# Kernel optimization log

Hardware: AMD Instinct MI355X
Metric: run time of the kernel (lower is better)

## Reference

```python
import jax, jax.numpy as jnp
import numpy as np

N_NODES = 100000
N_EDGES = 3200000
F_IN = 128
F_HID = 16
F_OUT = 1


def setup_inputs() -> dict:
    key = jax.random.key(0)
    ks = jax.random.split(key, 8)
    x = jax.random.normal(ks[0], (N_NODES, F_IN), dtype=jnp.float32)
    src = jax.random.randint(ks[1], (N_EDGES,), 0, N_NODES, dtype=jnp.int32)
    dst = jax.random.randint(ks[2], (N_EDGES,), 0, N_NODES, dtype=jnp.int32)
    edge_w = jax.random.uniform(ks[3], (N_EDGES,), dtype=jnp.float32)
    W0 = jax.random.normal(ks[4], (F_IN, F_HID), dtype=jnp.float32) / np.sqrt(F_IN)
    b0 = jnp.zeros((F_HID,), dtype=jnp.float32)
    W1 = jax.random.normal(ks[5], (F_HID, F_OUT), dtype=jnp.float32) / np.sqrt(F_HID)
    b1 = jnp.zeros((F_OUT,), dtype=jnp.float32)
    return {"x": x, "src": src, "dst": dst, "edge_w": edge_w,
            "W0": W0, "b0": b0, "W1": W1, "b1": b1}


def _spmm(src, dst, edge_w, h):
    # sparse A (COO) @ dense h: gather rows at src, weight, scatter-add to dst
    msgs = h[src] * edge_w[:, None]            # [E, F]
    return jax.ops.segment_sum(msgs, dst, num_segments=N_NODES)  # [N, F]


def reference(x, src, dst, edge_w, W0, b0, W1, b1):
    # GCNConv layer 0: relu(A @ (x @ W0) + b0)
    z0 = x @ W0                                 # [N, 16] linear transform first
    h = jax.nn.relu(_spmm(src, dst, edge_w, z0) + b0)
    # (Dropout is identity at inference)
    # GCNConv layer 1: sigmoid(A @ (h @ W1) + b1)
    z1 = h @ W1                                 # [N, 1]
    out = jax.nn.sigmoid(_spmm(src, dst, edge_w, z1) + b1)
    return out
```

## Files before the change

kernel.cpp:

```cpp
#include <hip/hip_runtime.h>

#define N_NODES 100000
#define N_EDGES 3200000
#define F_IN 128
#define F_HID 16

#define BK_LG 7
#define BK_NODES 128
#define NB ((N_NODES + BK_NODES - 1) / BK_NODES)
#define BCAPF 4736
#define CLG 10
#define CNODES 1024
#define NBC ((N_NODES + CNODES - 1) / CNODES)
#define NBC_P 128
#define BCAPC 34816
#define CPB2 9
#define CHUNK2 4096
#define CHUNK1 2048
#define NCH1 ((N_EDGES + CHUNK1 - 1) / CHUNK1)
#define NXB ((N_NODES + 63) / 64)
#define CUR_STRIDE 16

__device__ __forceinline__ unsigned short f2bf_rne(float f) {
    unsigned u = __float_as_uint(f);
    u += 0x7FFFu + ((u >> 16) & 1u);
    return (unsigned short)(u >> 16);
}

__global__ __launch_bounds__(256) void k_pre(const float* __restrict__ x,
                                             const float* __restrict__ W0,
                                             unsigned short* __restrict__ z0b,
                                             const int* __restrict__ src,
                                             const int* __restrict__ dst,
                                             const float* __restrict__ ew,
                                             int* __restrict__ cursorC,
                                             int2* __restrict__ ebinC) {
    __shared__ __align__(16) char smem[24832];
    const int tid = threadIdx.x;

    if ((blockIdx.x & 1) == 0) {
        const int xb = blockIdx.x >> 1;
        if (xb >= NXB) return;
        unsigned short* xsb = (unsigned short*)smem;
        float* w0s = (float*)(smem + 16640);
        for (int i = tid; i < F_IN * F_HID; i += 256) w0s[i] = W0[i];
        const int row0 = xb * 64;
        for (int i = tid; i < 64 * 32; i += 256) {
            int r = i >> 5, c4 = i & 31;
            float4 v = make_float4(0.f, 0.f, 0.f, 0.f);
            int row = row0 + r;
            if (row < N_NODES) v = ((const float4*)(x + (size_t)row * F_IN))[c4];
            *(ushort2*)(xsb + r * 130 + c4 * 4)     = make_ushort2(f2bf_rne(v.x), f2bf_rne(v.y));
            *(ushort2*)(xsb + r * 130 + c4 * 4 + 2) = make_ushort2(f2bf_rne(v.z), f2bf_rne(v.w));
        }
        __syncthreads();
        const int r  = tid & 63;
        const int cg = tid >> 6;
        float a0 = 0.f, a1 = 0.f, a2 = 0.f, a3 = 0.f;
        #pragma unroll 4
        for (int k = 0; k < F_IN; k += 2) {
            unsigned u = *(const unsigned*)(xsb + r * 130 + k);
            float xv0 = __uint_as_float(u << 16);
            float xv1 = __uint_as_float(u & 0xFFFF0000u);
            const float* wr0 = w0s + k * F_HID + cg * 4;
            const float* wr1 = wr0 + F_HID;
            a0 = fmaf(xv0, wr0[0], a0); a1 = fmaf(xv0, wr0[1], a1);
            a2 = fmaf(xv0, wr0[2], a2); a3 = fmaf(xv0, wr0[3], a3);
            a0 = fmaf(xv1, wr1[0], a0); a1 = fmaf(xv1, wr1[1], a1);
            a2 = fmaf(xv1, wr1[2], a2); a3 = fmaf(xv1, wr1[3], a3);
        }
        int row = row0 + r;
        if (row < N_NODES) {
            ushort4 p = make_ushort4(f2bf_rne(a0), f2bf_rne(a1),
                                     f2bf_rne(a2), f2bf_rne(a3));
            *(ushort4*)(z0b + (size_t)row * F_HID + cg * 4) = p;
        }
    } else {
        const int ch = blockIdx.x >> 1;
        if (ch >= NCH1) return;
        int2* stage = (int2*)smem;
        unsigned char* sbid = (unsigned char*)(smem + 16384);
        int* cnt  = (int*)(smem + 18432);
        int* excl = (int*)(smem + 18944);
        int* run  = (int*)(smem + 19456);
        int* gb   = (int*)(smem + 19968);
        int* alw  = (int*)(smem + 20480);
        int* wtot = (int*)(smem + 20992);
        const int e0  = ch * CHUNK1;
        const int nch = min(CHUNK1, N_EDGES - e0);

        for (int i = tid; i < NBC_P; i += 256) cnt[i] = 0;
        __syncthreads();

        const int EPT1 = CHUNK1 / 256;
        int es[8], eb[8], edl[8]; float ww[8];
        #pragma unroll
        for (int k = 0; k < EPT1; ++k) {
            int idx = k * 256 + tid;
            if (idx < nch) {
                int e = e0 + idx;
                int d = dst[e];
                es[k]  = src[e];
                ww[k]  = ew[e];
                eb[k]  = d >> CLG;
                edl[k] = d & (CNODES - 1);
                atomicAdd(&cnt[eb[k]], 1);
            } else {
                eb[k] = -1;
            }
        }
        __syncthreads();

        {
            const int lane = tid & 63;
            int inc = 0, dv_ = 0;
            if (tid < NBC_P) {
                dv_ = cnt[tid];
                inc = dv_;
                #pragma unroll
                for (int off = 1; off < 64; off <<= 1) {
                    int t = __shfl_up(inc, off);
                    if (lane >= off) inc += t;
                }
                if (lane == 63) wtot[tid >> 6] = inc;
            }
            __syncthreads();
            if (tid < NBC_P) {
                int base = (tid >= 64) ? wtot[0] : 0;
                excl[tid] = base + inc - dv_;
            }
        }
        __syncthreads();

        if (tid < NBC) {
            int c = cnt[tid];
            if (c > 0) {
                int old = atomicAdd(&cursorC[tid * CUR_STRIDE], c);
                int a = BCAPC - old;
                a = (a < 0) ? 0 : ((a > c) ? c : a);
                alw[tid] = a;
                gb[tid]  = tid * BCAPC + old;
            } else {
                alw[tid] = 0;
                gb[tid]  = tid * BCAPC;
            }
            run[tid] = 0;
        }
        __syncthreads();

        #pragma unroll
        for (int k = 0; k < EPT1; ++k) {
            if (eb[k] >= 0) {
                int b = eb[k];
                int p = excl[b] + atomicAdd(&run[b], 1);
                stage[p] = make_int2(__float_as_int(ww[k]), es[k] | (edl[k] << 17));
                sbid[p]  = (unsigned char)b;
            }
        }
        __syncthreads();

        for (int s = tid; s < nch; s += 256) {
            int b   = sbid[s];
            int off = s - excl[b];
            if (off < alw[b]) ebinC[(size_t)gb[b] + off] = stage[s];
        }
    }
}

__global__ __launch_bounds__(512) void k_bin2(const int* __restrict__ cursorC,
                                              const int2* __restrict__ ebinC,
                                              int* __restrict__ cursorF,
                                              int2* __restrict__ ebinF,
                                              int* __restrict__ deg) {
    __shared__ int cntw[64], runw[64], base[64];
    __shared__ int totals[8], excl_s[8], gb8[8], alw8[8];
    __shared__ int dcnt[CNODES];
    __shared__ int2 stage[CHUNK2];
    __shared__ unsigned char sbid[CHUNK2];
    const int tid = threadIdx.x;
    const int wid = tid >> 6;
    const int c   = blockIdx.x / CPB2;
    const int ck  = blockIdx.x % CPB2;
    const int ecnt = min(cursorC[c * CUR_STRIDE], BCAPC);
    const int beg  = ck * CHUNK2;
    const int n2   = min(CHUNK2, ecnt - beg);
    if (n2 <= 0) return;
    const int2* eC = ebinC + (size_t)c * BCAPC + beg;

    if (tid < 64) { cntw[tid] = 0; runw[tid] = 0; }
    for (int i = tid; i < CNODES; i += 512) dcnt[i] = 0;
    __syncthreads();

    const int EPT2 = CHUNK2 / 512;
    int fid[8]; int2 pk[8];
    #pragma unroll
    for (int k = 0; k < EPT2; ++k) {
        int idx = k * 512 + tid;
        if (idx < n2) {
            int2 e = eC[idx];
            int dlc = e.y >> 17;
            int f   = dlc >> BK_LG;
            fid[k]  = f;
            pk[k]   = make_int2(e.x, (e.y & 0x1FFFF) | ((dlc & (BK_NODES - 1)) << 17));
            atomicAdd(&cntw[f * 8 + wid], 1);
            atomicAdd(&dcnt[dlc], 1);
        } else {
            fid[k] = -1;
        }
    }
    __syncthreads();

    if (tid < 8) {
        int t = 0;
        #pragma unroll
        for (int w = 0; w < 8; ++w) t += cntw[tid * 8 + w];
        totals[tid] = t;
    }
    __syncthreads();
    if (tid < 8) {
        int e = 0;
        for (int f = 0; f < 8; ++f) if (f < tid) e += totals[f];
        excl_s[tid] = e;
        int t = totals[tid];
        int fb = c * 8 + tid;
        if (t > 0 && fb < NB) {
            int old = atomicAdd(&cursorF[fb * CUR_STRIDE], t);
            int a = BCAPF - old;
            a = (a < 0) ? 0 : ((a > t) ? t : a);
            alw8[tid] = a;
            gb8[tid]  = fb * BCAPF + old;
        } else {
            alw8[tid] = 0;
            gb8[tid]  = 0;
        }
    }
    __syncthreads();
    if (tid < 64) {
        int f = tid >> 3, w = tid & 7;
        int bb = excl_s[f];
        for (int w2 = 0; w2 < 8; ++w2) if (w2 < w) bb += cntw[f * 8 + w2];
        base[tid] = bb;
    }
    __syncthreads();

    #pragma unroll
    for (int k = 0; k < EPT2; ++k) {
        if (fid[k] >= 0) {
            int slot = fid[k] * 8 + wid;
            int p = base[slot] + atomicAdd(&runw[slot], 1);
            stage[p] = pk[k];
            sbid[p]  = (unsigned char)fid[k];
        }
    }
    __syncthreads();

    for (int s = tid; s < n2; s += 512) {
        int f   = sbid[s];
        int off = s - excl_s[f];
        if (off < alw8[f]) ebinF[(size_t)gb8[f] + off] = stage[s];
    }

    for (int i = tid; i < CNODES; i += 512) {
        int d = dcnt[i];
        int v = c * CNODES + i;
        if (d > 0 && v < N_NODES) atomicAdd(&deg[v], d);
    }
}

__global__ __launch_bounds__(512) void k_sg0(const int* __restrict__ deg,
                                             const int2* __restrict__ ebinF,
                                             const unsigned short* __restrict__ z0b,
                                             const float* __restrict__ b0,
                                             const float* __restrict__ W1,
                                             float* __restrict__ z1) {
    __shared__ int2 sorted[BCAPF];
    __shared__ int scn[BK_NODES], dg[BK_NODES], run[BK_NODES];
    __shared__ int wtot[2], ecnt_s;
    __shared__ float b0s[16], w1s[16];
    const int tid  = threadIdx.x;
    const int lane = tid & 63, wid = tid >> 6;
    const int b    = blockIdx.x;
    if (tid < 16) { b0s[tid] = b0[tid]; w1s[tid] = W1[tid]; }

    int inc = 0, d_ = 0;
    if (tid < BK_NODES) {
        int v = b * BK_NODES + tid;
        d_ = (v < N_NODES) ? deg[v] : 0;
        dg[tid]  = d_;
        run[tid] = 0;
        inc = d_;
        #pragma unroll
        for (int off = 1; off < 64; off <<= 1) {
            int t = __shfl_up(inc, off);
            if (lane >= off) inc += t;
        }
        if (lane == 63) wtot[tid >> 6] = inc;
    }
    __syncthreads();
    if (tid < BK_NODES) {
        int base = (tid >= 64) ? wtot[0] : 0;
        scn[tid] = base + inc - d_;
        if (tid == BK_NODES - 1) ecnt_s = min(base + inc, BCAPF);
    }
    __syncthreads();

    const int ecnt = ecnt_s;
    const int2* eb = ebinF + (size_t)b * BCAPF;
    for (int i = tid; i < ecnt; i += 512) {
        int2 e  = eb[i];
        int  dl = e.y >> 17;
        int  p  = scn[dl] + atomicAdd(&run[dl], 1);
        if (p < BCAPF) sorted[p] = e;
    }
    __syncthreads();

    for (int n = wid; n < BK_NODES; n += 8) {
        const int v = b * BK_NODES + n;
        if (v >= N_NODES) continue;
        const int beg = scn[n];
        const int end = min(beg + dg[n], BCAPF);
        const int dv  = end - beg;
        const int f2  = lane & 7;
        const int g   = lane >> 3;
        float acc0 = 0.f, acc1 = 0.f;
        for (int j = g; j < dv; j += 16) {
            int2 e0 = sorted[beg + j];
            int  j1 = j + 8;
            int2 e1 = (j1 < dv) ? sorted[beg + j1] : make_int2(0, 0);
            unsigned u0 = *(const unsigned*)(z0b + (size_t)(e0.y & 0x1FFFF) * F_HID + f2 * 2);
            unsigned u1 = *(const unsigned*)(z0b + (size_t)(e1.y & 0x1FFFF) * F_HID + f2 * 2);
            float w0 = __int_as_float(e0.x), w1 = __int_as_float(e1.x);
            acc0 = fmaf(__uint_as_float(u0 << 16),         w0, acc0);
            acc1 = fmaf(__uint_as_float(u0 & 0xFFFF0000u), w0, acc1);
            acc0 = fmaf(__uint_as_float(u1 << 16),         w1, acc0);
            acc1 = fmaf(__uint_as_float(u1 & 0xFFFF0000u), w1, acc1);
        }
        acc0 += __shfl_xor(acc0, 8);  acc1 += __shfl_xor(acc1, 8);
        acc0 += __shfl_xor(acc0, 16); acc1 += __shfl_xor(acc1, 16);
        acc0 += __shfl_xor(acc0, 32); acc1 += __shfl_xor(acc1, 32);
        float cc = fmaxf(acc0 + b0s[f2 * 2], 0.f) * w1s[f2 * 2]
                 + fmaxf(acc1 + b0s[f2 * 2 + 1], 0.f) * w1s[f2 * 2 + 1];
        cc += __shfl_xor(cc, 1);
        cc += __shfl_xor(cc, 2);
        cc += __shfl_xor(cc, 4);
        if (lane == 0) z1[v] = cc;
    }
}

__global__ __launch_bounds__(256) void k_g1(const int* __restrict__ cursorF,
                                            const int2* __restrict__ ebinF,
                                            const float* __restrict__ z1,
                                            const float* __restrict__ b1,
                                            float* __restrict__ out) {
    __shared__ float acc[BK_NODES];
    const int tid = threadIdx.x;
    const int b   = blockIdx.x;
    if (tid < BK_NODES) acc[tid] = 0.f;
    __syncthreads();
    const int   ecnt = min(cursorF[b * CUR_STRIDE], BCAPF);
    const int2* eb   = ebinF + (size_t)b * BCAPF;
    for (int i = tid; i < ecnt; i += 512) {
        int2 e0 = eb[i];
        int  i1 = i + 256;
        int2 e1 = (i1 < ecnt) ? eb[i1] : make_int2(0, 0);
        float m0 = z1[e0.y & 0x1FFFF] * __int_as_float(e0.x);
        float m1 = z1[e1.y & 0x1FFFF] * __int_as_float(e1.x);
        atomicAdd(&acc[e0.y >> 17], m0);
        if (i1 < ecnt) atomicAdd(&acc[e1.y >> 17], m1);
    }
    __syncthreads();
    if (tid < BK_NODES) {
        int v = b * BK_NODES + tid;
        if (v < N_NODES) out[v] = 1.f / (1.f + expf(-(acc[tid] + b1[0])));
    }
}

extern "C" void kernel_launch(void* const* d_in, const int* in_sizes, int n_in,
                              void* d_out, int out_size, void* d_ws, size_t ws_size,
                              hipStream_t stream) {
    const float* x   = (const float*)d_in[0];
    const int*   src = (const int*)d_in[1];
    const int*   dst = (const int*)d_in[2];
    const float* ew  = (const float*)d_in[3];
    const float* W0  = (const float*)d_in[4];
    const float* b0  = (const float*)d_in[5];
    const float* W1  = (const float*)d_in[6];
    const float* b1  = (const float*)d_in[7];
    float* out = (float*)d_out;

    unsigned short* z0b = (unsigned short*)d_ws;
    float* z1      = (float*)(z0b + (size_t)N_NODES * F_HID);
    int*   deg     = (int*)(z1 + N_NODES);
    int*   cursorC = deg + N_NODES;
    int*   cursorF = cursorC + NBC * CUR_STRIDE;
    int2*  ebinC   = (int2*)(cursorF + NB * CUR_STRIDE);
    int2*  ebinF   = ebinC + (size_t)NBC * BCAPC;

    hipMemsetAsync(deg, 0,
                   ((size_t)N_NODES + (size_t)(NBC + NB) * CUR_STRIDE) * sizeof(int),
                   stream);

    k_pre <<<2 * NCH1, 256, 0, stream>>>(x, W0, z0b, src, dst, ew, cursorC, ebinC);
    k_bin2<<<NBC * CPB2, 512, 0, stream>>>(cursorC, ebinC, cursorF, ebinF, deg);
    k_sg0 <<<NB, 512, 0, stream>>>(deg, ebinF, z0b, b0, W1, z1);
    k_g1  <<<NB, 256, 0, stream>>>(cursorF, ebinF, z1, b1, out);
}
```

Baseline: 135.4 us.

## Move x@W0 transform from first binning pass into second binning kernel

```diff
diff --git a/kernel.cpp b/kernel.cpp
--- a/kernel.cpp
+++ b/kernel.cpp
@@ -14,11 +14,14 @@
 #define NBC ((N_NODES + CNODES - 1) / CNODES)
 #define NBC_P 128
 #define BCAPC 34816
-#define CPB2 9
-#define CHUNK2 4096
 #define CHUNK1 2048
 #define NCH1 ((N_EDGES + CHUNK1 - 1) / CHUNK1)
+#define CHUNKM 2048
+#define CPB2 ((BCAPC + CHUNKM - 1) / CHUNKM)
+#define NMB (NBC * CPB2)
 #define NXB ((N_NODES + 63) / 64)
+#define PAIRED (2 * NXB)
+#define GRID_MID (NMB + NXB)
 #define CUR_STRIDE 16
 
 __device__ __forceinline__ unsigned short f2bf_rne(float f) {
@@ -27,24 +30,115 @@
     return (unsigned short)(u >> 16);
 }
 
-__global__ __launch_bounds__(256) void k_pre(const float* __restrict__ x,
+__global__ __launch_bounds__(256) void k_bin1(const int* __restrict__ src,
+                                              const int* __restrict__ dst,
+                                              const float* __restrict__ ew,
+                                              int* __restrict__ cursorC,
+                                              int2* __restrict__ ebinC) {
+    __shared__ int2 stage[CHUNK1];
+    __shared__ unsigned char sbid[CHUNK1];
+    __shared__ int cnt[NBC_P], excl[NBC_P], run[NBC_P], gb[NBC_P], alw[NBC_P];
+    __shared__ int wtot[2];
+    const int tid = threadIdx.x;
+    const int e0  = blockIdx.x * CHUNK1;
+    const int nch = min(CHUNK1, N_EDGES - e0);
+
+    for (int i = tid; i < NBC_P; i += 256) cnt[i] = 0;
+    __syncthreads();
+
+    int es[8], eb[8], edl[8]; float ww[8];
+    #pragma unroll
+    for (int k = 0; k < 8; ++k) {
+        int idx = k * 256 + tid;
+        if (idx < nch) {
+            int e = e0 + idx;
+            int d = dst[e];
+            es[k]  = src[e];
+            ww[k]  = ew[e];
+            eb[k]  = d >> CLG;
+            edl[k] = d & (CNODES - 1);
+            atomicAdd(&cnt[eb[k]], 1);
+        } else {
+            eb[k] = -1;
+        }
+    }
+    __syncthreads();
+
+    {
+        const int lane = tid & 63;
+        int inc = 0, dv_ = 0;
+        if (tid < NBC_P) {
+            dv_ = cnt[tid];
+            inc = dv_;
+            #pragma unroll
+            for (int off = 1; off < 64; off <<= 1) {
+                int t = __shfl_up(inc, off);
+                if (lane >= off) inc += t;
+            }
+            if (lane == 63) wtot[tid >> 6] = inc;
+        }
+        __syncthreads();
+        if (tid < NBC_P) {
+            int base = (tid >= 64) ? wtot[0] : 0;
+            excl[tid] = base + inc - dv_;
+        }
+    }
+    __syncthreads();
+
+    if (tid < NBC) {
+        int c = cnt[tid];
+        if (c > 0) {
+            int old = atomicAdd(&cursorC[tid * CUR_STRIDE], c);
+            int a = BCAPC - old;
+            a = (a < 0) ? 0 : ((a > c) ? c : a);
+            alw[tid] = a;
+            gb[tid]  = tid * BCAPC + old;
+        } else {
+            alw[tid] = 0;
+            gb[tid]  = tid * BCAPC;
+        }
+        run[tid] = 0;
+    }
+    __syncthreads();
+
+    #pragma unroll
+    for (int k = 0; k < 8; ++k) {
+        if (eb[k] >= 0) {
+            int b = eb[k];
+            int p = excl[b] + atomicAdd(&run[b], 1);
+            stage[p] = make_int2(__float_as_int(ww[k]), es[k] | (edl[k] << 17));
+            sbid[p]  = (unsigned char)b;
+        }
+    }
+    __syncthreads();
+
+    for (int s = tid; s < nch; s += 256) {
+        int b   = sbid[s];
+        int off = s - excl[b];
+        if (off < alw[b]) ebinC[(size_t)gb[b] + off] = stage[s];
+    }
+}
+
+__global__ __launch_bounds__(256) void k_mid(const int* __restrict__ cursorC,
+                                             const int2* __restrict__ ebinC,
+                                             int* __restrict__ cursorF,
+                                             int2* __restrict__ ebinF,
+                                             int* __restrict__ deg,
+                                             const float* __restrict__ x,
                                              const float* __restrict__ W0,
-                                             unsigned short* __restrict__ z0b,
-                                             const int* __restrict__ src,
-                                             const int* __restrict__ dst,
-                                             const float* __restrict__ ew,
-                                             int* __restrict__ cursorC,
-                                             int2* __restrict__ ebinC) {
+                                             unsigned short* __restrict__ z0b) {
     __shared__ __align__(16) char smem[24832];
     const int tid = threadIdx.x;
-
-    if ((blockIdx.x & 1) == 0) {
-        const int xb = blockIdx.x >> 1;
-        if (xb >= NXB) return;
+    const int bid = blockIdx.x;
+    int rid; bool isBin;
+    if (bid < PAIRED) { isBin = (bid & 1) == 0; rid = bid >> 1; }
+    else              { isBin = true; rid = NXB + (bid - PAIRED); }
+
+    if (!isBin) {
         unsigned short* xsb = (unsigned short*)smem;
         float* w0s = (float*)(smem + 16640);
         for (int i = tid; i < F_IN * F_HID; i += 256) w0s[i] = W0[i];
-        const int row0 = xb * 64;
+        const int row0 = rid * 64;
         for (int i = tid; i < 64 * 32; i += 256) {
             int r = i >> 5, c4 = i & 31;
             float4 v = make_float4(0.f, 0.f, 0.f, 0.f);
@@ -76,194 +170,102 @@
             *(ushort4*)(z0b + (size_t)row * F_HID + cg * 4) = p;
         }
     } else {
-        const int ch = blockIdx.x >> 1;
-        if (ch >= NCH1) return;
         int2* stage = (int2*)smem;
         unsigned char* sbid = (unsigned char*)(smem + 16384);
-        int* cnt  = (int*)(smem + 18432);
-        int* excl = (int*)(smem + 18944);
-        int* run  = (int*)(smem + 19456);
-        int* gb   = (int*)(smem + 19968);
-        int* alw  = (int*)(smem + 20480);
-        int* wtot = (int*)(smem + 20992);
-        const int e0  = ch * CHUNK1;
-        const int nch = min(CHUNK1, N_EDGES - e0);
-
-        for (int i = tid; i < NBC_P; i += 256) cnt[i] = 0;
-        __syncthreads();
-
-        const int EPT1 = CHUNK1 / 256;
-        int es[8], eb[8], edl[8]; float ww[8];
+        int* dcnt   = (int*)(smem + 18432);
+        int* cntw   = (int*)(smem + 22528);
+        int* runw   = (int*)(smem + 22656);
+        int* base   = (int*)(smem + 22784);
+        int* totals = (int*)(smem + 23040);
+        int* excl_s = (int*)(smem + 23072);
+        int* gb8    = (int*)(smem + 23104);
+        int* alw8   = (int*)(smem + 23136);
+        const int wid = tid >> 6;
+        const int c   = rid / CPB2;
+        const int ck  = rid % CPB2;
+        const int ecnt = min(cursorC[c * CUR_STRIDE], BCAPC);
+        const int beg  = ck * CHUNKM;
+        const int n2   = min(CHUNKM, ecnt - beg);
+        if (n2 <= 0) return;
+        const int2* eC = ebinC + (size_t)c * BCAPC + beg;
+
+        if (tid < 32) { cntw[tid] = 0; runw[tid] = 0; }
+        for (int i = tid; i < CNODES; i += 256) dcnt[i] = 0;
+        __syncthreads();
+
+        int fid[8]; int2 pk[8];
         #pragma unroll
-        for (int k = 0; k < EPT1; ++k) {
+        for (int k = 0; k < 8; ++k) {
             int idx = k * 256 + tid;
-            if (idx < nch) {
-                int e = e0 + idx;
-                int d = dst[e];
-                es[k]  = src[e];
-                ww[k]  = ew[e];
-                eb[k]  = d >> CLG;
-                edl[k] = d & (CNODES - 1);
-                atomicAdd(&cnt[eb[k]], 1);
+            if (idx < n2) {
+                int2 e = eC[idx];
+                int dlc = e.y >> 17;
+                int f   = dlc >> BK_LG;
+                fid[k]  = f;
+                pk[k]   = make_int2(e.x, (e.y & 0x1FFFF) | ((dlc & (BK_NODES - 1)) << 17));
+                atomicAdd(&cntw[f * 4 + wid], 1);
+                atomicAdd(&dcnt[dlc], 1);
             } else {
-                eb[k] = -1;
+                fid[k] = -1;
             }
         }
         __syncthreads();
 
-        {
-            const int lane = tid & 63;
-            int inc = 0, dv_ = 0;
-            if (tid < NBC_P) {
-                dv_ = cnt[tid];
-                inc = dv_;
-                #pragma unroll
-                for (int off = 1; off < 64; off <<= 1) {
-                    int t = __shfl_up(inc, off);
-                    if (lane >= off) inc += t;
-                }
-                if (lane == 63) wtot[tid >> 6] = inc;
+        if (tid < 8) {
+            int t = 0;
+            #pragma unroll
+            for (int w = 0; w < 4; ++w) t += cntw[tid * 4 + w];
+            totals[tid] = t;
+        }
+        __syncthreads();
+        if (tid < 8) {
+            int e = 0;
+            for (int f = 0; f < 8; ++f) if (f < tid) e += totals[f];
+            excl_s[tid] = e;
+            int t = totals[tid];
+            int fb = c * 8 + tid;
+            if (t > 0 && fb < NB) {
+                int old = atomicAdd(&cursorF[fb * CUR_STRIDE], t);
+                int a = BCAPF - old;
+                a = (a < 0) ? 0 : ((a > t) ? t : a);
+                alw8[tid] = a;
+                gb8[tid]  = fb * BCAPF + old;
+            } else {
+                alw8[tid] = 0;
+                gb8[tid]  = 0;
             }
-            __syncthreads();
-            if (tid < NBC_P) {
-                int base = (tid >= 64) ? wtot[0] : 0;
-                excl[tid] = base + inc - dv_;
+        }
+        __syncthreads();
+        if (tid < 32) {
+            int f = tid >> 2, w = tid & 3;
+            int bb = excl_s[f];
+            for (int w2 = 0; w2 < 4; ++w2) if (w2 < w) bb += cntw[f * 4 + w2];
+            base[tid] = bb;
+        }
+        __syncthreads();
+
+        #pragma unroll
+        for (int k = 0; k < 8; ++k) {
+            if (fid[k] >= 0) {
+                int slot = fid[k] * 4 + wid;
+                int p = base[slot] + atomicAdd(&runw[slot], 1);
+                stage[p] = pk[k];
+                sbid[p]  = (unsigned char)fid[k];
             }
         }
         __syncthreads();
 
-        if (tid < NBC) {
-            int c = cnt[tid];
-            if (c > 0) {
-                int old = atomicAdd(&cursorC[tid * CUR_STRIDE], c);
-                int a = BCAPC - old;
-                a = (a < 0) ? 0 : ((a > c) ? c : a);
-                alw[tid] = a;
-                gb[tid]  = tid * BCAPC + old;
-            } else {
-                alw[tid] = 0;
-                gb[tid]  = tid * BCAPC;
-            }
-            run[tid] = 0;
-        }
-        __syncthreads();
-
-        #pragma unroll
-        for (int k = 0; k < EPT1; ++k) {
-            if (eb[k] >= 0) {
-                int b = eb[k];
-                int p = excl[b] + atomicAdd(&run[b], 1);
-                stage[p] = make_int2(__float_as_int(ww[k]), es[k] | (edl[k] << 17));
-                sbid[p]  = (unsigned char)b;
-            }
-        }
-        __syncthreads();
-
-        for (int s = tid; s < nch; s += 256) {
-            int b   = sbid[s];
-            int off = s - excl[b];
-            if (off < alw[b]) ebinC[(size_t)gb[b] + off] = stage[s];
-        }
-    }
-}
-
-__global__ __launch_bounds__(512) void k_bin2(const int* __restrict__ cursorC,
-                                              const int2* __restrict__ ebinC,
-                                              int* __restrict__ cursorF,
-                                              int2* __restrict__ ebinF,
-                                              int* __restrict__ deg) {
-    __shared__ int cntw[64], runw[64], base[64];
-    __shared__ int totals[8], excl_s[8], gb8[8], alw8[8];
-    __shared__ int dcnt[CNODES];
-    __shared__ int2 stage[CHUNK2];
-    __shared__ unsigned char sbid[CHUNK2];
-    const int tid = threadIdx.x;
-    const int wid = tid >> 6;
-    const int c   = blockIdx.x / CPB2;
-    const int ck  = blockIdx.x % CPB2;
-    const int ecnt = min(cursorC[c * CUR_STRIDE], BCAPC);
-    const int beg  = ck * CHUNK2;
-    const int n2   = min(CHUNK2, ecnt - beg);
-    if (n2 <= 0) return;
-    const int2* eC = ebinC + (size_t)c * BCAPC + beg;
-
-    if (tid < 64) { cntw[tid] = 0; runw[tid] = 0; }
-    for (int i = tid; i < CNODES; i += 512) dcnt[i] = 0;
-    __syncthreads();
-
-    const int EPT2 = CHUNK2 / 512;
-    int fid[8]; int2 pk[8];
-    #pragma unroll
-    for (int k = 0; k < EPT2; ++k) {
-        int idx = k * 512 + tid;
-        if (idx < n2) {
-            int2 e = eC[idx];
-            int dlc = e.y >> 17;
-            int f   = dlc >> BK_LG;
-            fid[k]  = f;
-            pk[k]   = make_int2(e.x, (e.y & 0x1FFFF) | ((dlc & (BK_NODES - 1)) << 17));
-            atomicAdd(&cntw[f * 8 + wid], 1);
-            atomicAdd(&dcnt[dlc], 1);
-        } else {
-            fid[k] = -1;
-        }
-    }
-    __syncthreads();
-
-    if (tid < 8) {
-        int t = 0;
-        #pragma unroll
-        for (int w = 0; w < 8; ++w) t += cntw[tid * 8 + w];
-        totals[tid] = t;
-    }
-    __syncthreads();
-    if (tid < 8) {
-        int e = 0;
-        for (int f = 0; f < 8; ++f) if (f < tid) e += totals[f];
-        excl_s[tid] = e;
-        int t = totals[tid];
-        int fb = c * 8 + tid;
-        if (t > 0 && fb < NB) {
-            int old = atomicAdd(&cursorF[fb * CUR_STRIDE], t);
-            int a = BCAPF - old;
-            a = (a < 0) ? 0 : ((a > t) ? t : a);
-            alw8[tid] = a;
-            gb8[tid]  = fb * BCAPF + old;
-        } else {
-            alw8[tid] = 0;
-            gb8[tid]  = 0;
-        }
-    }
-    __syncthreads();
-    if (tid < 64) {
-        int f = tid >> 3, w = tid & 7;
-        int bb = excl_s[f];
-        for (int w2 = 0; w2 < 8; ++w2) if (w2 < w) bb += cntw[f * 8 + w2];
-        base[tid] = bb;
-    }
-    __syncthreads();
-
-    #pragma unroll
-    for (int k = 0; k < EPT2; ++k) {
-        if (fid[k] >= 0) {
-            int slot = fid[k] * 8 + wid;
-            int p = base[slot] + atomicAdd(&runw[slot], 1);
-            stage[p] = pk[k];
-            sbid[p]  = (unsigned char)fid[k];
-        }
-    }
-    __syncthreads();
-
-    for (int s = tid; s < n2; s += 512) {
-        int f   = sbid[s];
-        int off = s - excl_s[f];
-        if (off < alw8[f]) ebinF[(size_t)gb8[f] + off] = stage[s];
-    }
-
-    for (int i = tid; i < CNODES; i += 512) {
-        int d = dcnt[i];
-        int v = c * CNODES + i;
-        if (d > 0 && v < N_NODES) atomicAdd(&deg[v], d);
+        for (int s = tid; s < n2; s += 256) {
+            int f   = sbid[s];
+            int off = s - excl_s[f];
+            if (off < alw8[f]) ebinF[(size_t)gb8[f] + off] = stage[s];
+        }
+
+        for (int i = tid; i < CNODES; i += 256) {
+            int d = dcnt[i];
+            int v = c * CNODES + i;
+            if (d > 0 && v < N_NODES) atomicAdd(&deg[v], d);
+        }
     }
 }
 
@@ -400,8 +402,9 @@
                    ((size_t)N_NODES + (size_t)(NBC + NB) * CUR_STRIDE) * sizeof(int),
                    stream);
 
-    k_pre <<<2 * NCH1, 256, 0, stream>>>(x, W0, z0b, src, dst, ew, cursorC, ebinC);
-    k_bin2<<<NBC * CPB2, 512, 0, stream>>>(cursorC, ebinC, cursorF, ebinF, deg);
+    k_bin1<<<NCH1, 256, 0, stream>>>(src, dst, ew, cursorC, ebinC);
+    k_mid <<<GRID_MID, 256, 0, stream>>>(cursorC, ebinC, cursorF, ebinF, deg,
+                                         x, W0, z0b);
     k_sg0 <<<NB, 512, 0, stream>>>(deg, ebinF, z0b, b0, W1, z1);
     k_g1  <<<NB, 256, 0, stream>>>(cursorF, ebinF, z1, b1, out);
 }
```

New measurement: 137.6 us. Within noise of the previous version (+1.6%).
